# Kernel optimization log

Hardware: AMD Instinct MI355X
Metric: run time of the kernel (lower is better)

Reference implementation:

```python
import jax, jax.numpy as jnp
import numpy as np

NNZ = 16777216  # 2**24 nonzeros
D = 2048        # dense size (D, D, D); sum over dim 2 -> (D, D)


def setup_inputs() -> dict:
    key = jax.random.key(0)
    kv, ki = jax.random.split(key)
    values = jax.random.normal(kv, (NNZ,), dtype=jnp.float32)
    indices = jax.random.randint(ki, (3, NNZ), 0, D, dtype=jnp.int64)
    return {"values": values, "indices": indices}


def reference(values, indices):
    # sparse_coo_tensor(indices, values, size=(D,D,D)) -> sparse.sum(dim=2) -> to_dense()
    # is equivalent to a scatter-add of values keyed by (indices[0], indices[1]):
    # the third index only distinguishes entries that get summed away, and COO
    # coalescing already sums duplicate coordinates.
    out = jnp.zeros((D, D), dtype=jnp.float32)
    out = out.at[indices[0], indices[1]].add(values)
    return out
```

## Files before the change

### kernel.cpp

```cpp
#include <hip/hip_runtime.h>

#define NNZ 16777216
#define D 2048
#define NB 256
#define ROWS_PER_B 8
#define T1 512
#define EPT 16
#define CHUNK 8192
#define NCHUNK (NNZ / CHUNK)
#define SEG 8960
#define T2 1024
#define NW (T2 / 64)
#define RUNS (NCHUNK / NW)

__global__ __launch_bounds__(T1) void bin_scatter(
    const float* __restrict__ values,
    const int* __restrict__ idx0,
    const int* __restrict__ idx1,
    unsigned int* __restrict__ dump,
    unsigned int* __restrict__ pptabT)
{
    __shared__ unsigned int lhist[NB];
    __shared__ unsigned int ppref[NB];
    __shared__ unsigned int wsum[4];
    __shared__ unsigned int stage[SEG];

    const int tid = threadIdx.x;
    if (tid < NB) lhist[tid] = 0;
    __syncthreads();

    const int vecBase = blockIdx.x * (CHUNK / 4);

    float4 v[4]; int4 a[4]; int4 c[4];
#pragma unroll
    for (int it = 0; it < 4; ++it) {
        int g = vecBase + it * T1 + tid;
        v[it] = reinterpret_cast<const float4*>(values)[g];
        a[it] = reinterpret_cast<const int4*>(idx0)[g];
        c[it] = reinterpret_cast<const int4*>(idx1)[g];
    }

    unsigned int outw[EPT];
    unsigned int meta[EPT];
#pragma unroll
    for (int it = 0; it < 4; ++it) {
        const int*   ap = reinterpret_cast<const int*>(&a[it]);
        const int*   cp = reinterpret_cast<const int*>(&c[it]);
        const float* vp = reinterpret_cast<const float*>(&v[it]);
#pragma unroll
        for (int e = 0; e < 4; ++e) {
            int i0 = ap[e], i1 = cp[e];
            unsigned int b = (unsigned int)i0 >> 3;
            unsigned int fb = __float_as_uint(vp[e]);
            unsigned int bf = (fb + 0x7fffu + ((fb >> 16) & 1u)) >> 16;
            outw[it * 4 + e] = ((((unsigned int)(i0 & 7) << 11) | (unsigned int)i1) << 16) | bf;
            unsigned int rk = atomicAdd(&lhist[b], 1u);
            meta[it * 4 + e] = (b << 16) | rk;
        }
    }
    __syncthreads();

    unsigned int x = 0, pc = 0, cnt = 0;
    if (tid < NB) {
        const int lane = tid & 63;
        cnt = lhist[tid];
        pc = (cnt + 3u) & ~3u;
        x = pc;
#pragma unroll
        for (int dlt = 1; dlt < 64; dlt <<= 1) {
            unsigned int y = __shfl_up(x, dlt, 64);
            if (lane >= dlt) x += y;
        }
        if (lane == 63) wsum[tid >> 6] = x;
    }
    __syncthreads();
    if (tid < NB) {
        const int wid = tid >> 6;
        unsigned int off = 0;
#pragma unroll
        for (int w = 0; w < 4; ++w) off += (w < wid) ? wsum[w] : 0u;
        unsigned int excl = x - pc + off;
        ppref[tid] = excl;
        pptabT[(size_t)tid * NCHUNK + blockIdx.x] = (excl << 16) | cnt;
    }
    __syncthreads();

#pragma unroll
    for (int e = 0; e < EPT; ++e) {
        unsigned int b  = meta[e] >> 16;
        unsigned int rk = meta[e] & 0xFFFFu;
        stage[ppref[b] + rk] = outw[e];
    }
    __syncthreads();

    const uint4* s4 = reinterpret_cast<const uint4*>(stage);
    uint4* d4 = reinterpret_cast<uint4*>(dump + (size_t)blockIdx.x * SEG);
    for (int j = tid; j < SEG / 4; j += T1)
        d4[j] = s4[j];
}

__global__ __launch_bounds__(T2) void bucket_accumulate(
    const unsigned int* __restrict__ dump,
    const unsigned int* __restrict__ pptabT,
    float* __restrict__ out)
{
    __shared__ float tile[ROWS_PER_B * D];
    __shared__ unsigned int sdesc[NCHUNK];

    const int b = blockIdx.x;
    const int tid = threadIdx.x;
    const int w = tid >> 6;
    const int lane = tid & 63;

    for (int j = tid; j < ROWS_PER_B * D / 4; j += T2)
        reinterpret_cast<float4*>(tile)[j] = make_float4(0.f, 0.f, 0.f, 0.f);
    for (int j = tid; j < NCHUNK; j += T2)
        sdesc[j] = pptabT[(size_t)b * NCHUNK + j];
    __syncthreads();

    for (int j = tid; j < NCHUNK; j += T2) {
        unsigned int d = sdesc[j];
        unsigned int c = d & 0xFFFFu;
        if (c > 64u) {
            const unsigned int* base = dump + (unsigned int)j * SEG + (d >> 16);
            for (unsigned int t = 64u; t < c; ++t) {
                unsigned int ww = base[t];
                if (ww) atomicAdd(&tile[ww >> 16], __uint_as_float(ww << 16));
            }
        }
    }

    const unsigned int k0 = (unsigned int)w * RUNS;

#define PAYLOAD(kn, dsc) \
    ((lane < (int)((dsc) & 0xFFFFu)) \
        ? dump[(unsigned int)(kn) * SEG + ((dsc) >> 16) + (unsigned int)lane] : 0u)
#define ACC(wdv) if (wdv) atomicAdd(&tile[(wdv) >> 16], __uint_as_float((wdv) << 16));

    unsigned int wd0, wd1, wd2, wd3, wd4, wd5, wd6, wd7;
    {
        uint4 qa = *reinterpret_cast<const uint4*>(&sdesc[k0]);
        uint4 qb = *reinterpret_cast<const uint4*>(&sdesc[k0 + 4]);
        wd0 = PAYLOAD(k0 + 0, qa.x); wd1 = PAYLOAD(k0 + 1, qa.y);
        wd2 = PAYLOAD(k0 + 2, qa.z); wd3 = PAYLOAD(k0 + 3, qa.w);
        wd4 = PAYLOAD(k0 + 4, qb.x); wd5 = PAYLOAD(k0 + 5, qb.y);
        wd6 = PAYLOAD(k0 + 6, qb.z); wd7 = PAYLOAD(k0 + 7, qb.w);
    }

    for (int j = 0; j < RUNS; j += 8) {
        unsigned int nd0 = 0, nd1 = 0, nd2 = 0, nd3 = 0,
                     nd4 = 0, nd5 = 0, nd6 = 0, nd7 = 0;
        if (j + 8 < RUNS) {
            uint4 na = *reinterpret_cast<const uint4*>(&sdesc[k0 + j + 8]);
            uint4 nb = *reinterpret_cast<const uint4*>(&sdesc[k0 + j + 12]);
            nd0 = na.x; nd1 = na.y; nd2 = na.z; nd3 = na.w;
            nd4 = nb.x; nd5 = nb.y; nd6 = nb.z; nd7 = nb.w;
        }
        ACC(wd0) wd0 = PAYLOAD(k0 + j + 8,  nd0);
        ACC(wd1) wd1 = PAYLOAD(k0 + j + 9,  nd1);
        ACC(wd2) wd2 = PAYLOAD(k0 + j + 10, nd2);
        ACC(wd3) wd3 = PAYLOAD(k0 + j + 11, nd3);
        ACC(wd4) wd4 = PAYLOAD(k0 + j + 12, nd4);
        ACC(wd5) wd5 = PAYLOAD(k0 + j + 13, nd5);
        ACC(wd6) wd6 = PAYLOAD(k0 + j + 14, nd6);
        ACC(wd7) wd7 = PAYLOAD(k0 + j + 15, nd7);
    }
#undef ACC
#undef PAYLOAD
    __syncthreads();

    float4* o4 = reinterpret_cast<float4*>(out + (size_t)b * ROWS_PER_B * D);
    for (int j = tid; j < ROWS_PER_B * D / 4; j += T2)
        o4[j] = reinterpret_cast<float4*>(tile)[j];
}

__global__ __launch_bounds__(256) void scatter_add_kernel(
    const float* __restrict__ values,
    const int* __restrict__ idx0,
    const int* __restrict__ idx1,
    float* __restrict__ out)
{
    const int nvec = NNZ / 4;
    int tid = blockIdx.x * blockDim.x + threadIdx.x;
    int stride = gridDim.x * blockDim.x;
    for (int i = tid; i < nvec; i += stride) {
        const float4 v = reinterpret_cast<const float4*>(values)[i];
        const int4   a = reinterpret_cast<const int4*>(idx0)[i];
        const int4   b = reinterpret_cast<const int4*>(idx1)[i];
        atomicAdd(&out[a.x * D + b.x], v.x);
        atomicAdd(&out[a.y * D + b.y], v.y);
        atomicAdd(&out[a.z * D + b.z], v.z);
        atomicAdd(&out[a.w * D + b.w], v.w);
    }
}

extern "C" void kernel_launch(void* const* d_in, const int* in_sizes, int n_in,
                              void* d_out, int out_size, void* d_ws, size_t ws_size,
                              hipStream_t stream) {
    const float* values  = (const float*)d_in[0];
    const int*   indices = (const int*)d_in[1];
    const int*   idx0 = indices;
    const int*   idx1 = indices + NNZ;
    float* out = (float*)d_out;

    const size_t pp_bytes = (size_t)NB * NCHUNK * sizeof(unsigned int);
    const size_t need = pp_bytes + (size_t)NCHUNK * SEG * sizeof(unsigned int);

    if (ws_size < need) {
        hipMemsetAsync(out, 0, (size_t)out_size * sizeof(float), stream);
        const int nvec = NNZ / 4;
        scatter_add_kernel<<<(nvec + 255) / 256, 256, 0, stream>>>(values, idx0, idx1, out);
        return;
    }

    unsigned int* pptabT = (unsigned int*)d_ws;
    unsigned int* dump   = (unsigned int*)((char*)d_ws + pp_bytes);

    bin_scatter<<<NCHUNK, T1, 0, stream>>>(values, idx0, idx1, dump, pptabT);
    bucket_accumulate<<<NB, T2, 0, stream>>>(dump, pptabT, out);
}
```

Measured before the change: 146.8 us.

## Double chunk size per bin block and spread overflow accumulation across wave lanes

Doubles the per-block chunk in the binning kernel (32 elements per thread, larger staging segment), which halves the number of chunks and descriptors the accumulate kernel has to walk. The overflow path (buckets with more than 64 entries per chunk) now has each wave cooperate on one chunk with lane-strided loads instead of one thread looping serially. The main loop is restructured to peel the final iteration. It also adds an unused 16-bit shared array that is written but never read, which adds LDS pressure and stores, and the larger chunks will overflow 64 entries per bucket more often.

```diff
diff --git a/kernel.cpp b/kernel.cpp
--- a/kernel.cpp
+++ b/kernel.cpp
@@ -5,10 +5,10 @@
 #define NB 256
 #define ROWS_PER_B 8
 #define T1 512
-#define EPT 16
-#define CHUNK 8192
+#define EPT 32
+#define CHUNK 16384
 #define NCHUNK (NNZ / CHUNK)
-#define SEG 8960
+#define SEG 17152
 #define T2 1024
 #define NW (T2 / 64)
 #define RUNS (NCHUNK / NW)
@@ -23,7 +23,8 @@
     __shared__ unsigned int lhist[NB];
     __shared__ unsigned int ppref[NB];
     __shared__ unsigned int wsum[4];
-    __shared__ unsigned int stage[SEG];
+    __shared__ unsigned int skey[SEG];
+    __shared__ unsigned short sval[SEG];
 
     const int tid = threadIdx.x;
     if (tid < NB) lhist[tid] = 0;
@@ -31,9 +32,9 @@
 
     const int vecBase = blockIdx.x * (CHUNK / 4);
 
-    float4 v[4]; int4 a[4]; int4 c[4];
-#pragma unroll
-    for (int it = 0; it < 4; ++it) {
+    float4 v[8]; int4 a[8]; int4 c[8];
+#pragma unroll
+    for (int it = 0; it < 8; ++it) {
         int g = vecBase + it * T1 + tid;
         v[it] = reinterpret_cast<const float4*>(values)[g];
         a[it] = reinterpret_cast<const int4*>(idx0)[g];
@@ -43,7 +44,7 @@
     unsigned int outw[EPT];
     unsigned int meta[EPT];
 #pragma unroll
-    for (int it = 0; it < 4; ++it) {
+    for (int it = 0; it < 8; ++it) {
         const int*   ap = reinterpret_cast<const int*>(&a[it]);
         const int*   cp = reinterpret_cast<const int*>(&c[it]);
         const float* vp = reinterpret_cast<const float*>(&v[it]);
@@ -89,11 +90,13 @@
     for (int e = 0; e < EPT; ++e) {
         unsigned int b  = meta[e] >> 16;
         unsigned int rk = meta[e] & 0xFFFFu;
-        stage[ppref[b] + rk] = outw[e];
-    }
-    __syncthreads();
-
-    const uint4* s4 = reinterpret_cast<const uint4*>(stage);
+        unsigned int slot = ppref[b] + rk;
+        skey[slot] = outw[e];
+        sval[slot] = 0;
+    }
+    __syncthreads();
+
+    const uint4* s4 = reinterpret_cast<const uint4*>(skey);
     uint4* d4 = reinterpret_cast<uint4*>(dump + (size_t)blockIdx.x * SEG);
     for (int j = tid; j < SEG / 4; j += T1)
         d4[j] = s4[j];
@@ -118,14 +121,17 @@
         sdesc[j] = pptabT[(size_t)b * NCHUNK + j];
     __syncthreads();
 
-    for (int j = tid; j < NCHUNK; j += T2) {
-        unsigned int d = sdesc[j];
-        unsigned int c = d & 0xFFFFu;
-        if (c > 64u) {
-            const unsigned int* base = dump + (unsigned int)j * SEG + (d >> 16);
-            for (unsigned int t = 64u; t < c; ++t) {
-                unsigned int ww = base[t];
-                if (ww) atomicAdd(&tile[ww >> 16], __uint_as_float(ww << 16));
+    {
+        const int nwB = T2 / 64;
+        for (int j = w; j < NCHUNK; j += nwB) {
+            unsigned int d = sdesc[j];
+            unsigned int c = d & 0xFFFFu;
+            if (c > 64u) {
+                const unsigned int* base = dump + (unsigned int)j * SEG + (d >> 16);
+                for (unsigned int t = 64u + (unsigned)lane; t < c; t += 64u) {
+                    unsigned int ww = base[t];
+                    if (ww) atomicAdd(&tile[ww >> 16], __uint_as_float(ww << 16));
+                }
             }
         }
     }
@@ -147,24 +153,19 @@
         wd6 = PAYLOAD(k0 + 6, qb.z); wd7 = PAYLOAD(k0 + 7, qb.w);
     }
 
-    for (int j = 0; j < RUNS; j += 8) {
-        unsigned int nd0 = 0, nd1 = 0, nd2 = 0, nd3 = 0,
-                     nd4 = 0, nd5 = 0, nd6 = 0, nd7 = 0;
-        if (j + 8 < RUNS) {
-            uint4 na = *reinterpret_cast<const uint4*>(&sdesc[k0 + j + 8]);
-            uint4 nb = *reinterpret_cast<const uint4*>(&sdesc[k0 + j + 12]);
-            nd0 = na.x; nd1 = na.y; nd2 = na.z; nd3 = na.w;
-            nd4 = nb.x; nd5 = nb.y; nd6 = nb.z; nd7 = nb.w;
-        }
-        ACC(wd0) wd0 = PAYLOAD(k0 + j + 8,  nd0);
-        ACC(wd1) wd1 = PAYLOAD(k0 + j + 9,  nd1);
-        ACC(wd2) wd2 = PAYLOAD(k0 + j + 10, nd2);
-        ACC(wd3) wd3 = PAYLOAD(k0 + j + 11, nd3);
-        ACC(wd4) wd4 = PAYLOAD(k0 + j + 12, nd4);
-        ACC(wd5) wd5 = PAYLOAD(k0 + j + 13, nd5);
-        ACC(wd6) wd6 = PAYLOAD(k0 + j + 14, nd6);
-        ACC(wd7) wd7 = PAYLOAD(k0 + j + 15, nd7);
-    }
+    for (int j = 0; j < RUNS - 8; j += 8) {
+        uint4 na  = *reinterpret_cast<const uint4*>(&sdesc[k0 + j + 8]);
+        uint4 nb_ = *reinterpret_cast<const uint4*>(&sdesc[k0 + j + 12]);
+        ACC(wd0) wd0 = PAYLOAD(k0 + j + 8,  na.x);
+        ACC(wd1) wd1 = PAYLOAD(k0 + j + 9,  na.y);
+        ACC(wd2) wd2 = PAYLOAD(k0 + j + 10, na.z);
+        ACC(wd3) wd3 = PAYLOAD(k0 + j + 11, na.w);
+        ACC(wd4) wd4 = PAYLOAD(k0 + j + 12, nb_.x);
+        ACC(wd5) wd5 = PAYLOAD(k0 + j + 13, nb_.y);
+        ACC(wd6) wd6 = PAYLOAD(k0 + j + 14, nb_.z);
+        ACC(wd7) wd7 = PAYLOAD(k0 + j + 15, nb_.w);
+    }
+    ACC(wd0) ACC(wd1) ACC(wd2) ACC(wd3) ACC(wd4) ACC(wd5) ACC(wd6) ACC(wd7)
 #undef ACC
 #undef PAYLOAD
     __syncthreads();
```

New measurement: 164.9 us. 12.3% more time.
